# Optimization experiments

Measured on AMD Instinct MI355X. Metric: run time of the kernel, lower is better.

Reference implementation:

```python
import jax, jax.numpy as jnp
import numpy as np

OUT_RANGE = 6.0
OUT_SHIFT = -3.0


def setup_inputs() -> dict:
    key = jax.random.key(0)
    ks = jax.random.split(key, 6)
    B, T = 128, 64
    A, V, X = 48, 48, 96
    PF = 128
    fdim = (A + 1) * (V + 1) * (X + 1)  # 232897
    return {
        "audio_h": jax.random.normal(ks[0], (B, T, A), jnp.float32),
        "video_h": jax.random.normal(ks[1], (B, T, V), jnp.float32),
        "text_h": jax.random.normal(ks[2], (B, T, X), jnp.float32),
        "W1": jax.random.normal(ks[3], (fdim, PF), jnp.float32) * 0.002,
        "b1": jnp.zeros((PF,), jnp.float32),
        "W2": jax.random.normal(ks[4], (PF, PF), jnp.float32) * 0.05,
        "b2": jnp.zeros((PF,), jnp.float32),
        "W3": jax.random.normal(ks[5], (PF, 1), jnp.float32) * 0.05,
        "b3": jnp.zeros((1,), jnp.float32),
    }


def reference(audio_h, video_h, text_h, W1, b1, W2, b2, W3, b3):
    B, T, A = audio_h.shape
    V = video_h.shape[-1]
    X = text_h.shape[-1]
    one = jnp.ones((B, T, 1), audio_h.dtype)
    a = jnp.concatenate([one, audio_h], axis=-1)  # [B,T,A+1]
    v = jnp.concatenate([one, video_h], axis=-1)  # [B,T,V+1]
    x = jnp.concatenate([one, text_h], axis=-1)   # [B,T,X+1]
    # per-timestep triple outer product, summed over t.
    # flatten order matches torch: audio slowest, then video, text fastest.
    av = jnp.einsum("bta,btv->btav", a, v).reshape(B, T, (A + 1) * (V + 1))
    fusion = jnp.einsum("btp,btx->bpx", av, x).reshape(B, -1)  # [B,(A+1)(V+1)(X+1)]
    # dropout is identity in eval mode
    h1 = jax.nn.relu(fusion @ W1 + b1)
    h2 = jax.nn.relu(h1 @ W2 + b2)
    out = jax.nn.sigmoid(h2 @ W3 + b3) * OUT_RANGE + OUT_SHIFT  # [B,1] in (-3,3)
    return out
```

## Files before the change

kernel.cpp:

```cpp
#include <hip/hip_runtime.h>


#define B_    128
#define T_    64
#define A1    49
#define V1    49
#define X1    97
#define IJ    2401
#define KTOT  232897
#define FP    232928
#define PF    128
#define KC    512
#define NB2   455

typedef short s8v __attribute__((ext_vector_type(8)));
typedef float f4v __attribute__((ext_vector_type(4)));

__device__ __forceinline__ unsigned short f2bf(float f) {
    union { float f; unsigned u; } v; v.f = f;
    return (unsigned short)((v.u + 0x7FFFu + ((v.u >> 16) & 1u)) >> 16);
}

__global__ __launch_bounds__(512) void k1_fusion(
    const float* __restrict__ audio, const float* __restrict__ video,
    const float* __restrict__ text, unsigned short* __restrict__ fusion)
{
    __shared__ float a_s[T_ * A1];
    __shared__ float v_s[T_ * V1];
    __shared__ unsigned short xT[112 * 72];
    __shared__ unsigned short w_ws[8][16 * 72];

    const int b = blockIdx.y;
    const int bx = blockIdx.x;
    const int tid = threadIdx.x;

    for (int idx = tid; idx < T_ * A1; idx += 512) {
        int t = idx / 49, i = idx - t * 49;
        a_s[idx] = (i == 0) ? 1.0f : audio[(b * T_ + t) * 48 + (i - 1)];
        v_s[idx] = (i == 0) ? 1.0f : video[(b * T_ + t) * 48 + (i - 1)];
    }
    for (int idx = tid; idx < T_ * X1; idx += 512) {
        int t = idx / 97, k = idx - t * 97;
        xT[k * 72 + t] = f2bf((k == 0) ? 1.0f : text[(b * T_ + t) * 96 + (k - 1)]);
    }
    for (int idx = tid; idx < 15 * 64; idx += 512) {
        xT[(97 + (idx >> 6)) * 72 + (idx & 63)] = 0;
    }
    __syncthreads();

    const int wave = tid >> 6, lane = tid & 63;
    const int q = lane >> 4, ln = lane & 15;
    unsigned short* w_s = w_ws[wave];

    for (int it = 0; it < 5; ++it) {
        const int tw = it * 8 + wave;
        if (tw >= 38) break;
        const int tl = bx * 38 + tw;
        if (tl >= 151) break;
        const int ij0 = tl * 16;

        #pragma unroll
        for (int ijl = 0; ijl < 16; ++ijl) {
            int ij = ij0 + ijl;
            unsigned short wv = 0;
            if (ij < IJ) {
                int i = ij / 49, j = ij - i * 49;
                wv = f2bf(a_s[lane * 49 + i] * v_s[lane * 49 + j]);
            }
            w_s[ijl * 72 + lane] = wv;
        }
        s8v af0 = *(const s8v*)&w_s[ln * 72 + q * 8];
        s8v af1 = *(const s8v*)&w_s[ln * 72 + 32 + q * 8];
        #pragma unroll
        for (int nt = 0; nt < 7; ++nt) {
            s8v bf0 = *(const s8v*)&xT[(nt * 16 + ln) * 72 + q * 8];
            s8v bf1 = *(const s8v*)&xT[(nt * 16 + ln) * 72 + 32 + q * 8];
            f4v acc = {0.f, 0.f, 0.f, 0.f};
            acc = __builtin_amdgcn_mfma_f32_16x16x32_bf16(af0, bf0, acc, 0, 0, 0);
            acc = __builtin_amdgcn_mfma_f32_16x16x32_bf16(af1, bf1, acc, 0, 0, 0);
            int kk = nt * 16 + ln;
            if (kk < X1) {
                #pragma unroll
                for (int r = 0; r < 4; ++r) {
                    int ij = ij0 + q * 4 + r;
                    if (ij < IJ)
                        fusion[(size_t)b * FP + ij * X1 + kk] = f2bf(acc[r]);
                }
            }
        }
    }
}

__global__ __launch_bounds__(256) void k2_gemm(
    const unsigned short* __restrict__ fusion, const float* __restrict__ W1,
    float* __restrict__ partials)
{
    __shared__ unsigned short A_l[128 * 40];
    __shared__ unsigned short B_l[128 * 40];

    const int blk = blockIdx.x;
    const int kbase = blk * KC;
    const int nsteps = min(KC >> 5, (FP - kbase) >> 5);
    const int tid = threadIdx.x;
    const int wave = tid >> 6, lane = tid & 63;
    const int q = lane >> 4, ln = lane & 15;

    const int mA = tid >> 1, halfA = tid & 1;
    const int fB = tid & 127, gB = tid >> 7;

    f4v acc[2][8];
    for (int h = 0; h < 2; ++h)
        for (int n = 0; n < 8; ++n) acc[h][n] = (f4v){0.f, 0.f, 0.f, 0.f};

    for (int s = 0; s < nsteps; ++s) {
        const int p0 = kbase + s * 32;
        uint4 av0 = *(const uint4*)&fusion[(size_t)mA * FP + p0 + halfA * 16];
        uint4 av1 = *(const uint4*)&fusion[(size_t)mA * FP + p0 + halfA * 16 + 8];
        float bv[16];
        #pragma unroll
        for (int c = 0; c < 16; ++c) {
            int p = p0 + gB * 16 + c;
            bv[c] = (p < KTOT) ? W1[(size_t)p * PF + fB] : 0.f;
        }
        __syncthreads();
        *(uint4*)&A_l[mA * 40 + halfA * 16] = av0;
        *(uint4*)&A_l[mA * 40 + halfA * 16 + 8] = av1;
        #pragma unroll
        for (int c = 0; c < 4; ++c) {
            ushort4 pk;
            pk.x = f2bf(bv[c * 4 + 0]); pk.y = f2bf(bv[c * 4 + 1]);
            pk.z = f2bf(bv[c * 4 + 2]); pk.w = f2bf(bv[c * 4 + 3]);
            *(ushort4*)&B_l[fB * 40 + gB * 16 + c * 4] = pk;
        }
        __syncthreads();
        s8v a0 = *(const s8v*)&A_l[(wave * 32 + ln) * 40 + q * 8];
        s8v a1 = *(const s8v*)&A_l[(wave * 32 + 16 + ln) * 40 + q * 8];
        #pragma unroll
        for (int nt = 0; nt < 8; ++nt) {
            s8v bf = *(const s8v*)&B_l[(nt * 16 + ln) * 40 + q * 8];
            acc[0][nt] = __builtin_amdgcn_mfma_f32_16x16x32_bf16(a0, bf, acc[0][nt], 0, 0, 0);
            acc[1][nt] = __builtin_amdgcn_mfma_f32_16x16x32_bf16(a1, bf, acc[1][nt], 0, 0, 0);
        }
    }

    float* outp = partials + (size_t)blk * (128 * 128);
    for (int h = 0; h < 2; ++h) {
        int mrow = wave * 32 + h * 16 + q * 4;
        for (int nt = 0; nt < 8; ++nt) {
            int f = nt * 16 + ln;
            for (int r = 0; r < 4; ++r)
                outp[(mrow + r) * 128 + f] = acc[h][nt][r];
        }
    }
}

__global__ __launch_bounds__(256) void k3_reduce(
    const float* __restrict__ partials, const float* __restrict__ b1,
    float* __restrict__ h1)
{
    __shared__ float red[256];
    const int e = blockIdx.x * 64 + (threadIdx.x & 63);
    const int rh = threadIdx.x >> 6;
    float s = 0.f;
    for (int r = rh; r < NB2; r += 4)
        s += partials[(size_t)r * 16384 + e];
    red[threadIdx.x] = s;
    __syncthreads();
    if (threadIdx.x < 64) {
        float v = red[threadIdx.x] + red[threadIdx.x + 64] +
                  red[threadIdx.x + 128] + red[threadIdx.x + 192];
        v += b1[e & 127];
        h1[e] = fmaxf(v, 0.f);
    }
}

__global__ __launch_bounds__(128) void k4_mlp(
    const float* __restrict__ h1, const float* __restrict__ W2,
    const float* __restrict__ b2, float* __restrict__ h2)
{
    __shared__ float hrow[128];
    const int b = blockIdx.x, f = threadIdx.x;
    hrow[f] = h1[b * 128 + f];
    __syncthreads();
    float s = b2[f];
    #pragma unroll 8
    for (int c = 0; c < 128; ++c) s += hrow[c] * W2[c * 128 + f];
    h2[b * 128 + f] = fmaxf(s, 0.f);
}

__global__ __launch_bounds__(128) void k5_out(
    const float* __restrict__ h2, const float* __restrict__ W3,
    const float* __restrict__ b3, float* __restrict__ out)
{
    int b = threadIdx.x;
    float s = b3[0];
    for (int c = 0; c < 128; ++c) s += h2[b * 128 + c] * W3[c];
    out[b] = 6.0f / (1.0f + expf(-s)) - 3.0f;
}

extern "C" void kernel_launch(void* const* d_in, const int* in_sizes, int n_in,
                              void* d_out, int out_size, void* d_ws, size_t ws_size,
                              hipStream_t stream)
{
    const float* audio = (const float*)d_in[0];
    const float* video = (const float*)d_in[1];
    const float* text  = (const float*)d_in[2];
    const float* W1 = (const float*)d_in[3];
    const float* b1 = (const float*)d_in[4];
    const float* W2 = (const float*)d_in[5];
    const float* b2 = (const float*)d_in[6];
    const float* W3 = (const float*)d_in[7];
    const float* b3 = (const float*)d_in[8];
    float* out = (float*)d_out;

    char* ws = (char*)d_ws;
    unsigned short* fusion = (unsigned short*)ws;
    float* partials = (float*)(ws + 59629568);
    float* h1 = (float*)(ws + 89448448);
    float* h2 = (float*)(ws + 89513984);

    k1_fusion<<<dim3(4, 128), 512, 0, stream>>>(audio, video, text, fusion);
    k2_gemm<<<dim3(NB2), 256, 0, stream>>>(fusion, W1, partials);
    k3_reduce<<<dim3(256), 256, 0, stream>>>(partials, b1, h1);
    k4_mlp<<<dim3(128), 128, 0, stream>>>(h1, W2, b2, h2);
    k5_out<<<dim3(1), 128, 0, stream>>>(h2, W3, b3, out);
}
```

Before: 276.6 us.

## Double-buffer W1 tiles in split-K GEMM, load A directly to registers, fuse MLP tail

The split-K GEMM now runs 512 threads with one 16-row slice per wave. Each wave loads its fusion A fragment straight from global memory into registers, with no LDS staging. W1 tiles are double-buffered in LDS and the next step's loads are issued before the current MFMAs, leaving one barrier per step instead of two. The padding tail of fusion is zeroed so the unmasked A loads read zeros. The reduce kernel uses 512 threads, and the second and third MLP layers are fused into one kernel with a shuffle reduction, which removes a launch.

```diff
diff --git a/kernel.cpp b/kernel.cpp
--- a/kernel.cpp
+++ b/kernel.cpp
@@ -45,6 +45,10 @@
     }
     for (int idx = tid; idx < 15 * 64; idx += 512) {
         xT[(97 + (idx >> 6)) * 72 + (idx & 63)] = 0;
+    }
+    if (bx == 0) {
+        for (int idx = tid; idx < FP - KTOT; idx += 512)
+            fusion[(size_t)b * FP + KTOT + idx] = 0;
     }
     __syncthreads();
 
@@ -91,12 +95,12 @@
     }
 }
 
-__global__ __launch_bounds__(256) void k2_gemm(
+#define BPAD 40
+__global__ __launch_bounds__(512) void k2_gemm(
     const unsigned short* __restrict__ fusion, const float* __restrict__ W1,
     float* __restrict__ partials)
 {
-    __shared__ unsigned short A_l[128 * 40];
-    __shared__ unsigned short B_l[128 * 40];
+    __shared__ unsigned short B_l[2][128 * BPAD];
 
     const int blk = blockIdx.x;
     const int kbase = blk * KC;
@@ -105,97 +109,114 @@
     const int wave = tid >> 6, lane = tid & 63;
     const int q = lane >> 4, ln = lane & 15;
 
-    const int mA = tid >> 1, halfA = tid & 1;
-    const int fB = tid & 127, gB = tid >> 7;
-
-    f4v acc[2][8];
-    for (int h = 0; h < 2; ++h)
-        for (int n = 0; n < 8; ++n) acc[h][n] = (f4v){0.f, 0.f, 0.f, 0.f};
+    const int fB = tid & 127, g = tid >> 7;
+
+    const unsigned short* Arow =
+        fusion + (size_t)(wave * 16 + ln) * FP + kbase + q * 8;
+
+    f4v acc[8];
+    #pragma unroll
+    for (int n = 0; n < 8; ++n) acc[n] = (f4v){0.f, 0.f, 0.f, 0.f};
+
+    {
+        float bv[8];
+        #pragma unroll
+        for (int c = 0; c < 8; ++c) {
+            int p = kbase + g * 8 + c;
+            bv[c] = (p < KTOT) ? W1[(size_t)p * PF + fB] : 0.f;
+        }
+        ushort4 lo, hi;
+        lo.x = f2bf(bv[0]); lo.y = f2bf(bv[1]); lo.z = f2bf(bv[2]); lo.w = f2bf(bv[3]);
+        hi.x = f2bf(bv[4]); hi.y = f2bf(bv[5]); hi.z = f2bf(bv[6]); hi.w = f2bf(bv[7]);
+        *(ushort4*)&B_l[0][fB * BPAD + g * 8]     = lo;
+        *(ushort4*)&B_l[0][fB * BPAD + g * 8 + 4] = hi;
+    }
+    s8v av = *(const s8v*)Arow;
+    __syncthreads();
 
     for (int s = 0; s < nsteps; ++s) {
-        const int p0 = kbase + s * 32;
-        uint4 av0 = *(const uint4*)&fusion[(size_t)mA * FP + p0 + halfA * 16];
-        uint4 av1 = *(const uint4*)&fusion[(size_t)mA * FP + p0 + halfA * 16 + 8];
-        float bv[16];
-        #pragma unroll
-        for (int c = 0; c < 16; ++c) {
-            int p = p0 + gB * 16 + c;
-            bv[c] = (p < KTOT) ? W1[(size_t)p * PF + fB] : 0.f;
+        const int cbuf = s & 1, nbuf = cbuf ^ 1;
+        float bvn[8];
+        s8v avn;
+        const bool more = (s + 1 < nsteps);
+        if (more) {
+            const int p1 = kbase + (s + 1) * 32;
+            #pragma unroll
+            for (int c = 0; c < 8; ++c) {
+                int p = p1 + g * 8 + c;
+                bvn[c] = (p < KTOT) ? W1[(size_t)p * PF + fB] : 0.f;
+            }
+            avn = *(const s8v*)(Arow + (s + 1) * 32);
+        }
+        #pragma unroll
+        for (int nt = 0; nt < 8; ++nt) {
+            s8v bf = *(const s8v*)&B_l[cbuf][(nt * 16 + ln) * BPAD + q * 8];
+            acc[nt] = __builtin_amdgcn_mfma_f32_16x16x32_bf16(av, bf, acc[nt], 0, 0, 0);
+        }
+        if (more) {
+            ushort4 lo, hi;
+            lo.x = f2bf(bvn[0]); lo.y = f2bf(bvn[1]); lo.z = f2bf(bvn[2]); lo.w = f2bf(bvn[3]);
+            hi.x = f2bf(bvn[4]); hi.y = f2bf(bvn[5]); hi.z = f2bf(bvn[6]); hi.w = f2bf(bvn[7]);
+            *(ushort4*)&B_l[nbuf][fB * BPAD + g * 8]     = lo;
+            *(ushort4*)&B_l[nbuf][fB * BPAD + g * 8 + 4] = hi;
+            av = avn;
         }
         __syncthreads();
-        *(uint4*)&A_l[mA * 40 + halfA * 16] = av0;
-        *(uint4*)&A_l[mA * 40 + halfA * 16 + 8] = av1;
-        #pragma unroll
-        for (int c = 0; c < 4; ++c) {
-            ushort4 pk;
-            pk.x = f2bf(bv[c * 4 + 0]); pk.y = f2bf(bv[c * 4 + 1]);
-            pk.z = f2bf(bv[c * 4 + 2]); pk.w = f2bf(bv[c * 4 + 3]);
-            *(ushort4*)&B_l[fB * 40 + gB * 16 + c * 4] = pk;
-        }
-        __syncthreads();
-        s8v a0 = *(const s8v*)&A_l[(wave * 32 + ln) * 40 + q * 8];
-        s8v a1 = *(const s8v*)&A_l[(wave * 32 + 16 + ln) * 40 + q * 8];
-        #pragma unroll
-        for (int nt = 0; nt < 8; ++nt) {
-            s8v bf = *(const s8v*)&B_l[(nt * 16 + ln) * 40 + q * 8];
-            acc[0][nt] = __builtin_amdgcn_mfma_f32_16x16x32_bf16(a0, bf, acc[0][nt], 0, 0, 0);
-            acc[1][nt] = __builtin_amdgcn_mfma_f32_16x16x32_bf16(a1, bf, acc[1][nt], 0, 0, 0);
-        }
     }
 
     float* outp = partials + (size_t)blk * (128 * 128);
-    for (int h = 0; h < 2; ++h) {
-        int mrow = wave * 32 + h * 16 + q * 4;
-        for (int nt = 0; nt < 8; ++nt) {
-            int f = nt * 16 + ln;
-            for (int r = 0; r < 4; ++r)
-                outp[(mrow + r) * 128 + f] = acc[h][nt][r];
-        }
-    }
-}
-
-__global__ __launch_bounds__(256) void k3_reduce(
+    #pragma unroll
+    for (int nt = 0; nt < 8; ++nt) {
+        const int f = nt * 16 + ln;
+        #pragma unroll
+        for (int r = 0; r < 4; ++r)
+            outp[(wave * 16 + q * 4 + r) * 128 + f] = acc[nt][r];
+    }
+}
+
+__global__ __launch_bounds__(512) void k3_reduce(
     const float* __restrict__ partials, const float* __restrict__ b1,
     float* __restrict__ h1)
 {
-    __shared__ float red[256];
+    __shared__ float red[512];
     const int e = blockIdx.x * 64 + (threadIdx.x & 63);
     const int rh = threadIdx.x >> 6;
     float s = 0.f;
-    for (int r = rh; r < NB2; r += 4)
+    for (int r = rh; r < NB2; r += 8)
         s += partials[(size_t)r * 16384 + e];
     red[threadIdx.x] = s;
     __syncthreads();
     if (threadIdx.x < 64) {
-        float v = red[threadIdx.x] + red[threadIdx.x + 64] +
-                  red[threadIdx.x + 128] + red[threadIdx.x + 192];
+        float v = 0.f;
+        #pragma unroll
+        for (int j = 0; j < 8; ++j) v += red[threadIdx.x + 64 * j];
         v += b1[e & 127];
         h1[e] = fmaxf(v, 0.f);
     }
 }
 
-__global__ __launch_bounds__(128) void k4_mlp(
+__global__ __launch_bounds__(128) void k4_out(
     const float* __restrict__ h1, const float* __restrict__ W2,
-    const float* __restrict__ b2, float* __restrict__ h2)
+    const float* __restrict__ b2, const float* __restrict__ W3,
+    const float* __restrict__ b3, float* __restrict__ out)
 {
     __shared__ float hrow[128];
+    __shared__ float red2[2];
     const int b = blockIdx.x, f = threadIdx.x;
     hrow[f] = h1[b * 128 + f];
     __syncthreads();
     float s = b2[f];
     #pragma unroll 8
     for (int c = 0; c < 128; ++c) s += hrow[c] * W2[c * 128 + f];
-    h2[b * 128 + f] = fmaxf(s, 0.f);
-}
-
-__global__ __launch_bounds__(128) void k5_out(
-    const float* __restrict__ h2, const float* __restrict__ W3,
-    const float* __restrict__ b3, float* __restrict__ out)
-{
-    int b = threadIdx.x;
-    float s = b3[0];
-    for (int c = 0; c < 128; ++c) s += h2[b * 128 + c] * W3[c];
-    out[b] = 6.0f / (1.0f + expf(-s)) - 3.0f;
+    float p = fmaxf(s, 0.f) * W3[f];
+    #pragma unroll
+    for (int off = 32; off; off >>= 1) p += __shfl_down(p, off, 64);
+    if ((f & 63) == 0) red2[f >> 6] = p;
+    __syncthreads();
+    if (f == 0) {
+        float t = red2[0] + red2[1] + b3[0];
+        out[b] = 6.0f / (1.0f + expf(-t)) - 3.0f;
+    }
 }
 
 extern "C" void kernel_launch(void* const* d_in, const int* in_sizes, int n_in,
@@ -217,11 +238,9 @@
     unsigned short* fusion = (unsigned short*)ws;
     float* partials = (float*)(ws + 59629568);
     float* h1 = (float*)(ws + 89448448);
-    float* h2 = (float*)(ws + 89513984);
 
     k1_fusion<<<dim3(4, 128), 512, 0, stream>>>(audio, video, text, fusion);
-    k2_gemm<<<dim3(NB2), 256, 0, stream>>>(fusion, W1, partials);
-    k3_reduce<<<dim3(256), 256, 0, stream>>>(partials, b1, h1);
-    k4_mlp<<<dim3(128), 128, 0, stream>>>(h1, W2, b2, h2);
-    k5_out<<<dim3(1), 128, 0, stream>>>(h2, W3, b3, out);
-}
+    k2_gemm<<<dim3(NB2), 512, 0, stream>>>(fusion, W1, partials);
+    k3_reduce<<<dim3(256), 512, 0, stream>>>(partials, b1, h1);
+    k4_out<<<dim3(128), 128, 0, stream>>>(h1, W2, b2, W3, b3, out);
+}
```

Result: faster. 256.6 us (-7.2%).
